# Optimization experiments

Measured on AMD Instinct MI355X. Metric: run time of the kernel, lower is better.

## Reference

```python
import jax, jax.numpy as jnp
import numpy as np

B, L, R = 4, 2048, 1024        # batch, seq_len, residual_dim
HID, EXP, K = 64, 2, 3          # hidden_dim, expansion_factor, conv_kernel_size
D = HID * EXP                   # ssm_input_dim = 128
N = HID                         # SSM state size = 64


def setup_inputs() -> dict:
    key = jax.random.key(0)
    ks = jax.random.split(key, 16)
    g = lambda k, s: jax.random.normal(k, s, dtype=jnp.float32) * 0.02
    inp = {
        "up_x":   jax.random.normal(ks[0], (B, L, R), dtype=jnp.float32),
        "W_up":   g(ks[1], (R, 2 * D)),
        "b_up":   g(ks[2], (2 * D,)),
        "conv_w": g(ks[3], (D, K)),          # depthwise Conv1d weight [C,1,K] squeezed
        "conv_b": g(ks[4], (D,)),
        "W_delta": g(ks[5], (D, D)),
        "b_delta": g(ks[6], (D,)),
        "W_B":    g(ks[7], (D, N)),
        "b_B":    g(ks[8], (N,)),
        "W_C":    g(ks[9], (D, N)),
        "b_C":    g(ks[10], (N,)),
        "A_log":  jnp.log(jnp.broadcast_to(jnp.arange(1, N + 1, dtype=jnp.float32), (D, N))),
        "D_skip": jnp.ones((D,), dtype=jnp.float32),
        "W_down": g(ks[11], (D, R)),
        "b_down": g(ks[12], (R,)),
    }
    return inp


def reference(up_x, W_up, b_up, conv_w, conv_b, W_delta, b_delta,
              W_B, b_B, W_C, b_C, A_log, D_skip, W_down, b_down):
    Lq = up_x.shape[1]
    u = up_x @ W_up + b_up                               # [B,L,2D]
    left, right = jnp.split(u, 2, axis=-1)               # each [B,L,D]

    # causal depthwise conv (pad left K-1, truncate to L)
    xp = jnp.pad(left, ((0, 0), (K - 1, 0), (0, 0)))     # [B,L+K-1,D]
    conv = sum(conv_w[:, k] * xp[:, k:k + Lq, :] for k in range(K)) + conv_b
    x = jax.nn.silu(conv)                                # [B,L,D]

    # S6 selective scan
    delta = jax.nn.softplus(x @ W_delta + b_delta)       # [B,L,D]
    Bm = x @ W_B + b_B                                   # [B,L,N]
    Cm = x @ W_C + b_C                                   # [B,L,N]
    A = -jnp.exp(A_log)                                  # [D,N]
    dA = jnp.exp(delta[..., None] * A)                   # [B,L,D,N]
    dBx = delta[..., None] * Bm[:, :, None, :] * x[..., None]  # [B,L,D,N]

    def step(h, inputs):
        dA_t, dBx_t, C_t = inputs                        # [B,D,N],[B,D,N],[B,N]
        h = dA_t * h + dBx_t
        y_t = jnp.einsum('bdn,bn->bd', h, C_t)
        return h, y_t

    h0 = jnp.zeros((up_x.shape[0], D, N), dtype=x.dtype)
    _, ys = jax.lax.scan(step, h0, (jnp.swapaxes(dA, 0, 1),
                                    jnp.swapaxes(dBx, 0, 1),
                                    jnp.swapaxes(Cm, 0, 1)))
    y = jnp.swapaxes(ys, 0, 1) + D_skip * x              # [B,L,D]

    gated = y * jax.nn.silu(right)                       # SiLU gate
    return gated @ W_down + b_down                       # [B,L,R]
```

## Files before the change

### kernel.cpp

```cpp
#include <hip/hip_runtime.h>
#include <math.h>

#define B_ 4
#define L_ 2048
#define R_ 1024
#define D_ 128
#define N_ 64
#define TWO_D 256
#define M_ (B_*L_)

#define LNC 6
#define NC 64

#define LSTR 68
#define LSTRX 136

typedef __attribute__((ext_vector_type(8))) short bf16x8;
typedef __attribute__((ext_vector_type(4))) float f32x4;

__device__ __forceinline__ float silu_f(float z) {
    return z / (1.0f + __expf(-z));
}

__device__ __forceinline__ float softplus_f(float z) {
    return fmaxf(z, 0.0f) + log1pf(__expf(-fabsf(z)));
}

__device__ __forceinline__ short f2bf(float f) {
    union { float f; unsigned int u; } v; v.f = f;
    unsigned int r = v.u + 0x7FFF + ((v.u >> 16) & 1);
    return (short)(r >> 16);
}

__device__ __forceinline__ bf16x8 pack8(float4 a, float4 b) {
    bf16x8 r;
    r[0] = f2bf(a.x); r[1] = f2bf(a.y); r[2] = f2bf(a.z); r[3] = f2bf(a.w);
    r[4] = f2bf(b.x); r[5] = f2bf(b.y); r[6] = f2bf(b.z); r[7] = f2bf(b.w);
    return r;
}

__global__ __launch_bounds__(256) void gemm_up_splitk(
    const float* __restrict__ A,
    const float* __restrict__ W,
    float* __restrict__ P0,
    float* __restrict__ P1)
{
    __shared__ short Al[64 * LSTR];
    __shared__ short Bl[64 * LSTR];

    int lid = blockIdx.x;
    int xcd = lid & 7;
    int slot = lid >> 3;
    int bm = xcd * 16 + (slot >> 3);
    int r3 = slot & 7;
    int bn = r3 & 3;
    int split = r3 >> 2;
    float* P = split ? P1 : P0;
    int k0 = split * 512;

    int tid = threadIdx.x;
    int w = tid >> 6, l = tid & 63;
    int lm = l & 15, q = l >> 4;
    int wm = (w & 1) * 32, wn = (w >> 1) * 32;

    f32x4 acc00 = {0,0,0,0}, acc01 = {0,0,0,0}, acc10 = {0,0,0,0}, acc11 = {0,0,0,0};

    int ar = tid >> 2, ak = (tid & 3) * 8;
    int bcol = tid & 63, bk = (tid >> 6) * 8;

    const float* Ag = A + (size_t)(bm * 64 + ar) * 1024 + k0 + ak;
    const float* Wg = W + (size_t)k0 * TWO_D + (size_t)bn * 64 + bcol;

    for (int kt = 0; kt < 512; kt += 32) {
        float4 a0 = *(const float4*)(Ag + kt);
        float4 a1 = *(const float4*)(Ag + kt + 4);
        *(bf16x8*)&Al[ar * LSTR + ak] = pack8(a0, a1);

        float w0 = Wg[(size_t)(kt + bk + 0) * TWO_D];
        float w1 = Wg[(size_t)(kt + bk + 1) * TWO_D];
        float w2 = Wg[(size_t)(kt + bk + 2) * TWO_D];
        float w3 = Wg[(size_t)(kt + bk + 3) * TWO_D];
        float w4 = Wg[(size_t)(kt + bk + 4) * TWO_D];
        float w5 = Wg[(size_t)(kt + bk + 5) * TWO_D];
        float w6 = Wg[(size_t)(kt + bk + 6) * TWO_D];
        float w7 = Wg[(size_t)(kt + bk + 7) * TWO_D];
        *(bf16x8*)&Bl[bcol * LSTR + bk] =
            pack8(make_float4(w0, w1, w2, w3), make_float4(w4, w5, w6, w7));

        __syncthreads();

        bf16x8 af0 = *(bf16x8*)&Al[(wm + lm) * LSTR + q * 8];
        bf16x8 af1 = *(bf16x8*)&Al[(wm + 16 + lm) * LSTR + q * 8];
        bf16x8 bf0 = *(bf16x8*)&Bl[(wn + lm) * LSTR + q * 8];
        bf16x8 bf1 = *(bf16x8*)&Bl[(wn + 16 + lm) * LSTR + q * 8];

        acc00 = __builtin_amdgcn_mfma_f32_16x16x32_bf16(af0, bf0, acc00, 0, 0, 0);
        acc01 = __builtin_amdgcn_mfma_f32_16x16x32_bf16(af0, bf1, acc01, 0, 0, 0);
        acc10 = __builtin_amdgcn_mfma_f32_16x16x32_bf16(af1, bf0, acc10, 0, 0, 0);
        acc11 = __builtin_amdgcn_mfma_f32_16x16x32_bf16(af1, bf1, acc11, 0, 0, 0);

        __syncthreads();
    }

    #pragma unroll
    for (int i = 0; i < 4; i++) {
        int r0 = bm * 64 + wm + q * 4 + i;
        int r1 = r0 + 16;
        int c0 = bn * 64 + wn + lm;
        int c1 = c0 + 16;
        P[(size_t)r0 * TWO_D + c0] = acc00[i];
        P[(size_t)r0 * TWO_D + c1] = acc01[i];
        P[(size_t)r1 * TWO_D + c0] = acc10[i];
        P[(size_t)r1 * TWO_D + c1] = acc11[i];
    }
}

__global__ __launch_bounds__(256) void convproj_mfma(
    const float* __restrict__ P0,
    const float* __restrict__ P1,
    const float* __restrict__ b_up,
    const float* __restrict__ conv_w,
    const float* __restrict__ conv_b,
    const float* __restrict__ W_delta, const float* __restrict__ b_delta,
    const float* __restrict__ W_B,     const float* __restrict__ b_B,
    const float* __restrict__ W_C,     const float* __restrict__ b_C,
    float* __restrict__ x,
    float* __restrict__ u,
    float* __restrict__ delta,
    float* __restrict__ Bm,
    float* __restrict__ Cm)
{
    __shared__ float uu[66 * 128];
    __shared__ short Xl[64 * LSTRX];
    __shared__ short Bl[64 * LSTR];

    int lid = blockIdx.x;
    int xcd = lid & 7;
    int slot = lid >> 3;
    int bm = xcd * 16 + (slot >> 2);
    int bn = slot & 3;
    int tid = threadIdx.x;

    bool seq_start = (bm & 31) == 0;

    #pragma unroll
    for (int i = 0; i < 9; i++) {
        int fi = tid + i * 256;
        if (fi < 2112) {
            int row = fi >> 5;
            int c4 = (fi & 31) * 4;
            int gr = bm * 64 + row - 2;
            float4 v;
            if (seq_start && row < 2) {
                v = make_float4(0.f, 0.f, 0.f, 0.f);
            } else {
                size_t gi = (size_t)gr * TWO_D + c4;
                float4 p0 = *(const float4*)&P0[gi];
                float4 p1 = *(const float4*)&P1[gi];
                float4 bb = *(const float4*)&b_up[c4];
                v = make_float4(p0.x + p1.x + bb.x, p0.y + p1.y + bb.y,
                                p0.z + p1.z + bb.z, p0.w + p1.w + bb.w);
            }
            *(float4*)&uu[fi * 4] = v;
        }
    }

    if (bn == 1) {
        #pragma unroll
        for (int i = 0; i < 8; i++) {
            int fi = tid + i * 256;
            int row = fi >> 5;
            int c4 = (fi & 31) * 4 + 128;
            int gr = bm * 64 + row;
            size_t gi = (size_t)gr * TWO_D + c4;
            float4 p0 = *(const float4*)&P0[gi];
            float4 p1 = *(const float4*)&P1[gi];
            float4 bb = *(const float4*)&b_up[c4];
            *(float4*)&u[gi] = make_float4(p0.x + p1.x + bb.x, p0.y + p1.y + bb.y,
                                           p0.z + p1.z + bb.z, p0.w + p1.w + bb.w);
        }
    }
    __syncthreads();

    #pragma unroll
    for (int i = 0; i < 8; i++) {
        int fi = tid + i * 256;
        int row = fi >> 5;
        int c4 = (fi & 31) * 4;
        float4 v2 = *(const float4*)&uu[(row + 2) * 128 + c4];
        float4 v1 = *(const float4*)&uu[(row + 1) * 128 + c4];
        float4 v0 = *(const float4*)&uu[(row + 0) * 128 + c4];
        float4 z;
        {
            float w0 = conv_w[(c4 + 0) * 3 + 0], w1 = conv_w[(c4 + 0) * 3 + 1], w2 = conv_w[(c4 + 0) * 3 + 2];
            z.x = silu_f(fmaf(w0, v0.x, fmaf(w1, v1.x, fmaf(w2, v2.x, conv_b[c4 + 0]))));
        }
        {
            float w0 = conv_w[(c4 + 1) * 3 + 0], w1 = conv_w[(c4 + 1) * 3 + 1], w2 = conv_w[(c4 + 1) * 3 + 2];
            z.y = silu_f(fmaf(w0, v0.y, fmaf(w1, v1.y, fmaf(w2, v2.y, conv_b[c4 + 1]))));
        }
        {
            float w0 = conv_w[(c4 + 2) * 3 + 0], w1 = conv_w[(c4 + 2) * 3 + 1], w2 = conv_w[(c4 + 2) * 3 + 2];
            z.z = silu_f(fmaf(w0, v0.z, fmaf(w1, v1.z, fmaf(w2, v2.z, conv_b[c4 + 2]))));
        }
        {
            float w0 = conv_w[(c4 + 3) * 3 + 0], w1 = conv_w[(c4 + 3) * 3 + 1], w2 = conv_w[(c4 + 3) * 3 + 2];
            z.w = silu_f(fmaf(w0, v0.w, fmaf(w1, v1.w, fmaf(w2, v2.w, conv_b[c4 + 3]))));
        }
        short4 zb;
        zb.x = f2bf(z.x); zb.y = f2bf(z.y); zb.z = f2bf(z.z); zb.w = f2bf(z.w);
        *(short4*)&Xl[row * LSTRX + c4] = zb;
        if (bn == 0) {
            int gr = bm * 64 + row;
            *(float4*)&x[(size_t)gr * D_ + c4] = z;
        }
    }

    const float* Wsel; const float* bsel; int wstride;
    if (bn < 2)       { Wsel = W_delta + bn * 64; bsel = b_delta + bn * 64; wstride = 128; }
    else if (bn == 2) { Wsel = W_B;               bsel = b_B;               wstride = 64;  }
    else              { Wsel = W_C;               bsel = b_C;               wstride = 64;  }

    int w = tid >> 6, l = tid & 63;
    int lm = l & 15, q = l >> 4;
    int wm = (w & 1) * 32, wn = (w >> 1) * 32;

    f32x4 acc00 = {0,0,0,0}, acc01 = {0,0,0,0}, acc10 = {0,0,0,0}, acc11 = {0,0,0,0};

    int bcol = tid & 63, bk = (tid >> 6) * 8;
    const float* Wg = Wsel + bcol;

    __syncthreads();

    for (int kt = 0; kt < 128; kt += 32) {
        float w0 = Wg[(size_t)(kt + bk + 0) * wstride];
        float w1 = Wg[(size_t)(kt + bk + 1) * wstride];
        float w2 = Wg[(size_t)(kt + bk + 2) * wstride];
        float w3 = Wg[(size_t)(kt + bk + 3) * wstride];
        float w4 = Wg[(size_t)(kt + bk + 4) * wstride];
        float w5 = Wg[(size_t)(kt + bk + 5) * wstride];
        float w6 = Wg[(size_t)(kt + bk + 6) * wstride];
        float w7 = Wg[(size_t)(kt + bk + 7) * wstride];
        *(bf16x8*)&Bl[bcol * LSTR + bk] =
            pack8(make_float4(w0, w1, w2, w3), make_float4(w4, w5, w6, w7));

        __syncthreads();

        bf16x8 af0 = *(bf16x8*)&Xl[(wm + lm) * LSTRX + kt + q * 8];
        bf16x8 af1 = *(bf16x8*)&Xl[(wm + 16 + lm) * LSTRX + kt + q * 8];
        bf16x8 bf0 = *(bf16x8*)&Bl[(wn + lm) * LSTR + q * 8];
        bf16x8 bf1 = *(bf16x8*)&Bl[(wn + 16 + lm) * LSTR + q * 8];

        acc00 = __builtin_amdgcn_mfma_f32_16x16x32_bf16(af0, bf0, acc00, 0, 0, 0);
        acc01 = __builtin_amdgcn_mfma_f32_16x16x32_bf16(af0, bf1, acc01, 0, 0, 0);
        acc10 = __builtin_amdgcn_mfma_f32_16x16x32_bf16(af1, bf0, acc10, 0, 0, 0);
        acc11 = __builtin_amdgcn_mfma_f32_16x16x32_bf16(af1, bf1, acc11, 0, 0, 0);

        __syncthreads();
    }

    #pragma unroll
    for (int i = 0; i < 4; i++) {
        int r0 = bm * 64 + wm + q * 4 + i;
        int r1 = r0 + 16;
        int c0 = wn + lm;
        int c1 = c0 + 16;
        float v00 = acc00[i] + bsel[c0];
        float v01 = acc01[i] + bsel[c1];
        float v10 = acc10[i] + bsel[c0];
        float v11 = acc11[i] + bsel[c1];
        if (bn < 2) {
            int cc0 = bn * 64 + c0, cc1 = bn * 64 + c1;
            delta[(size_t)r0 * D_ + cc0] = softplus_f(v00);
            delta[(size_t)r0 * D_ + cc1] = softplus_f(v01);
            delta[(size_t)r1 * D_ + cc0] = softplus_f(v10);
            delta[(size_t)r1 * D_ + cc1] = softplus_f(v11);
        } else if (bn == 2) {
            Bm[(size_t)r0 * N_ + c0] = v00;
            Bm[(size_t)r0 * N_ + c1] = v01;
            Bm[(size_t)r1 * N_ + c0] = v10;
            Bm[(size_t)r1 * N_ + c1] = v11;
        } else {
            Cm[(size_t)r0 * N_ + c0] = v00;
            Cm[(size_t)r0 * N_ + c1] = v01;
            Cm[(size_t)r1 * N_ + c0] = v10;
            Cm[(size_t)r1 * N_ + c1] = v11;
        }
    }
}

__global__ __launch_bounds__(256) void scan_sumA(
    const float* __restrict__ delta,
    const float* __restrict__ x,
    const float* __restrict__ Bm,
    const float* __restrict__ A_log,
    float* __restrict__ ch_aprod,
    float* __restrict__ ch_h)
{
    constexpr int TCt = L_ >> LNC;

    int wid = blockIdx.x * 4 + (threadIdx.x >> 6);
    int l = threadIdx.x & 63;
    int g = l >> 4, j = l & 15;
    int c = wid & (NC - 1);
    int dq = (wid >> LNC) & 31;
    int b = wid >> (LNC + 5);
    int d = dq * 4 + g;

    const float LOG2E = 1.44269504089f;
    float4 Ar = *(const float4*)&A_log[d * N_ + j * 4];
    float Ai0 = -__expf(Ar.x) * LOG2E;
    float Ai1 = -__expf(Ar.y) * LOG2E;
    float Ai2 = -__expf(Ar.z) * LOG2E;
    float Ai3 = -__expf(Ar.w) * LOG2E;

    size_t row0 = (size_t)b * L_ + c * TCt;
    const float* dp = delta + row0 * D_ + d;
    const float* xp = x     + row0 * D_ + d;
    const float* bp = Bm    + row0 * N_ + j * 4;

    float h0 = 0, h1 = 0, h2 = 0, h3 = 0;
    float S = 0;

    #pragma unroll 8
    for (int t = 0; t < TCt; t++) {
        float dl = dp[t * D_];
        float xv = xp[t * D_];
        float4 bv = *(const float4*)&bp[t * N_];
        float e0 = exp2f(dl * Ai0);
        float e1 = exp2f(dl * Ai1);
        float e2 = exp2f(dl * Ai2);
        float e3 = exp2f(dl * Ai3);
        float dbx = dl * xv;
        h0 = fmaf(e0, h0, dbx * bv.x);
        h1 = fmaf(e1, h1, dbx * bv.y);
        h2 = fmaf(e2, h2, dbx * bv.z);
        h3 = fmaf(e3, h3, dbx * bv.w);
        S += dl;
    }

    size_t ci = (((size_t)b * D_ + d) * NC + c) * N_ + j * 4;
    *(float4*)&ch_aprod[ci] = make_float4(exp2f(Ai0 * S), exp2f(Ai1 * S),
                                          exp2f(Ai2 * S), exp2f(Ai3 * S));
    *(float4*)&ch_h[ci]     = make_float4(h0, h1, h2, h3);
}

__global__ __launch_bounds__(256) void scan_prefix(
    float* __restrict__ aprod_hin,
    const float* __restrict__ ch_h)
{
    int idx = blockIdx.x * 256 + threadIdx.x;
    int n = idx & 63;
    int rest = idx >> 6;
    size_t base = (size_t)rest * NC * N_ + n;
    float h = 0.0f;
    #pragma unroll 8
    for (int c = 0; c < NC; c++) {
        size_t o = base + (size_t)c * N_;
        float a  = aprod_hin[o];
        float hh = ch_h[o];
        aprod_hin[o] = h;
        h = fmaf(a, h, hh);
    }
}

__global__ __launch_bounds__(256) void scan_outB(
    const float* __restrict__ delta,
    const float* __restrict__ x,
    const float* __restrict__ Bm,
    const float* __restrict__ Cm,
    const float* __restrict__ A_log,
    const float* __restrict__ D_skip,
    const float* __restrict__ hin,
    float* __restrict__ y)
{
    constexpr int TCt = L_ >> LNC;

    int wid = blockIdx.x * 4 + (threadIdx.x >> 6);
    int l = threadIdx.x & 63;
    int g = l >> 4, j = l & 15;
    int c = wid & (NC - 1);
    int dq = (wid >> LNC) & 31;
    int b = wid >> (LNC + 5);
    int d = dq * 4 + g;

    const float LOG2E = 1.44269504089f;
    float4 Ar = *(const float4*)&A_log[d * N_ + j * 4];
    float Ai0 = -__expf(Ar.x) * LOG2E;
    float Ai1 = -__expf(Ar.y) * LOG2E;
    float Ai2 = -__expf(Ar.z) * LOG2E;
    float Ai3 = -__expf(Ar.w) * LOG2E;
    float dsk = D_skip[d];

    float4 hv = *(const float4*)&hin[(((size_t)b * D_ + d) * NC + c) * N_ + j * 4];
    float h0 = hv.x, h1 = hv.y, h2 = hv.z, h3 = hv.w;

    size_t row0 = (size_t)b * L_ + c * TCt;
    const float* dp = delta + row0 * D_ + d;
    const float* xp = x     + row0 * D_ + d;
    const float* bp = Bm    + row0 * N_ + j * 4;
    const float* cp = Cm    + row0 * N_ + j * 4;
    float*       yp = y     + row0 * D_ + d;

    #pragma unroll 8
    for (int t = 0; t < TCt; t++) {
        float dl = dp[t * D_];
        float xv = xp[t * D_];
        float4 bv = *(const float4*)&bp[t * N_];
        float4 cv = *(const float4*)&cp[t * N_];
        float e0 = exp2f(dl * Ai0);
        float e1 = exp2f(dl * Ai1);
        float e2 = exp2f(dl * Ai2);
        float e3 = exp2f(dl * Ai3);
        float dbx = dl * xv;
        h0 = fmaf(e0, h0, dbx * bv.x);
        h1 = fmaf(e1, h1, dbx * bv.y);
        h2 = fmaf(e2, h2, dbx * bv.z);
        h3 = fmaf(e3, h3, dbx * bv.w);
        float p = fmaf(h0, cv.x, fmaf(h1, cv.y, fmaf(h2, cv.z, h3 * cv.w)));
        p += __shfl_xor(p, 1, 64);
        p += __shfl_xor(p, 2, 64);
        p += __shfl_xor(p, 4, 64);
        p += __shfl_xor(p, 8, 64);
        if (j == 0) yp[t * D_] = fmaf(dsk, xv, p);
    }
}

__global__ __launch_bounds__(256) void gemm_down_mfma(
    const float* __restrict__ y,
    const float* __restrict__ u,
    const float* __restrict__ W,
    const float* __restrict__ bias,
    float* __restrict__ out)
{
    __shared__ short Al[64 * LSTR];
    __shared__ short Bl[64 * LSTR];

    int lid = blockIdx.x;
    int xcd = lid & 7;
    int slot = lid >> 3;
    int bm = xcd * 16 + (slot >> 4);
    int bn = slot & 15;

    int tid = threadIdx.x;
    int w = tid >> 6, l = tid & 63;
    int lm = l & 15, q = l >> 4;
    int wm = (w & 1) * 32, wn = (w >> 1) * 32;

    f32x4 acc00 = {0,0,0,0}, acc01 = {0,0,0,0}, acc10 = {0,0,0,0}, acc11 = {0,0,0,0};

    int ar = tid >> 2, ak = (tid & 3) * 8;
    int bcol = tid & 63, bk = (tid >> 6) * 8;

    const float* Yg = y + (size_t)(bm * 64 + ar) * D_ + ak;
    const float* Ug = u + (size_t)(bm * 64 + ar) * TWO_D + D_ + ak;
    const float* Wg = W + (size_t)bn * 64 + bcol;

    for (int kt = 0; kt < 128; kt += 32) {
        float4 y0 = *(const float4*)(Yg + kt);
        float4 y1 = *(const float4*)(Yg + kt + 4);
        float4 g0 = *(const float4*)(Ug + kt);
        float4 g1 = *(const float4*)(Ug + kt + 4);
        float4 a0 = make_float4(y0.x * silu_f(g0.x), y0.y * silu_f(g0.y),
                                y0.z * silu_f(g0.z), y0.w * silu_f(g0.w));
        float4 a1 = make_float4(y1.x * silu_f(g1.x), y1.y * silu_f(g1.y),
                                y1.z * silu_f(g1.z), y1.w * silu_f(g1.w));
        *(bf16x8*)&Al[ar * LSTR + ak] = pack8(a0, a1);

        float w0 = Wg[(size_t)(kt + bk + 0) * R_];
        float w1 = Wg[(size_t)(kt + bk + 1) * R_];
        float w2 = Wg[(size_t)(kt + bk + 2) * R_];
        float w3 = Wg[(size_t)(kt + bk + 3) * R_];
        float w4 = Wg[(size_t)(kt + bk + 4) * R_];
        float w5 = Wg[(size_t)(kt + bk + 5) * R_];
        float w6 = Wg[(size_t)(kt + bk + 6) * R_];
        float w7 = Wg[(size_t)(kt + bk + 7) * R_];
        *(bf16x8*)&Bl[bcol * LSTR + bk] =
            pack8(make_float4(w0, w1, w2, w3), make_float4(w4, w5, w6, w7));

        __syncthreads();

        bf16x8 af0 = *(bf16x8*)&Al[(wm + lm) * LSTR + q * 8];
        bf16x8 af1 = *(bf16x8*)&Al[(wm + 16 + lm) * LSTR + q * 8];
        bf16x8 bf0 = *(bf16x8*)&Bl[(wn + lm) * LSTR + q * 8];
        bf16x8 bf1 = *(bf16x8*)&Bl[(wn + 16 + lm) * LSTR + q * 8];

        acc00 = __builtin_amdgcn_mfma_f32_16x16x32_bf16(af0, bf0, acc00, 0, 0, 0);
        acc01 = __builtin_amdgcn_mfma_f32_16x16x32_bf16(af0, bf1, acc01, 0, 0, 0);
        acc10 = __builtin_amdgcn_mfma_f32_16x16x32_bf16(af1, bf0, acc10, 0, 0, 0);
        acc11 = __builtin_amdgcn_mfma_f32_16x16x32_bf16(af1, bf1, acc11, 0, 0, 0);

        __syncthreads();
    }

    #pragma unroll
    for (int i = 0; i < 4; i++) {
        int r0 = bm * 64 + wm + q * 4 + i;
        int r1 = r0 + 16;
        int c0 = bn * 64 + wn + lm;
        int c1 = c0 + 16;
        out[(size_t)r0 * R_ + c0] = acc00[i] + bias[c0];
        out[(size_t)r0 * R_ + c1] = acc01[i] + bias[c1];
        out[(size_t)r1 * R_ + c0] = acc10[i] + bias[c0];
        out[(size_t)r1 * R_ + c1] = acc11[i] + bias[c1];
    }
}

extern "C" void kernel_launch(void* const* d_in, const int* in_sizes, int n_in,
                              void* d_out, int out_size, void* d_ws, size_t ws_size,
                              hipStream_t stream)
{
    const float* up_x    = (const float*)d_in[0];
    const float* W_up    = (const float*)d_in[1];
    const float* b_up    = (const float*)d_in[2];
    const float* conv_w  = (const float*)d_in[3];
    const float* conv_b  = (const float*)d_in[4];
    const float* W_delta = (const float*)d_in[5];
    const float* b_delta = (const float*)d_in[6];
    const float* W_B     = (const float*)d_in[7];
    const float* b_B     = (const float*)d_in[8];
    const float* W_C     = (const float*)d_in[9];
    const float* b_C     = (const float*)d_in[10];
    const float* A_log   = (const float*)d_in[11];
    const float* D_skip  = (const float*)d_in[12];
    const float* W_down  = (const float*)d_in[13];
    const float* b_down  = (const float*)d_in[14];

    float* out = (float*)d_out;
    float* ws  = (float*)d_ws;

    float* u     = ws;
    float* x     = u + (size_t)M_ * TWO_D;
    float* delta = x + (size_t)M_ * D_;
    float* Bm    = delta + (size_t)M_ * D_;
    float* Cm    = Bm + (size_t)M_ * N_;
    float* y     = Cm + (size_t)M_ * N_;
    float* ch_aprod = y + (size_t)M_ * D_;
    float* ch_h  = ch_aprod + (size_t)B_ * D_ * NC * N_;
    float* P0    = ch_h + (size_t)B_ * D_ * NC * N_;
    float* P1    = P0 + (size_t)M_ * TWO_D;

    gemm_up_splitk<<<1024, 256, 0, stream>>>(up_x, W_up, P0, P1);

    convproj_mfma<<<512, 256, 0, stream>>>(
        P0, P1, b_up, conv_w, conv_b,
        W_delta, b_delta, W_B, b_B, W_C, b_C,
        x, u, delta, Bm, Cm);

    scan_sumA<<<(B_ * (D_ / 4) * NC) / 4, 256, 0, stream>>>(
        delta, x, Bm, A_log, ch_aprod, ch_h);
    scan_prefix<<<(B_ * D_ * N_) / 256, 256, 0, stream>>>(
        ch_aprod, ch_h);
    scan_outB<<<(B_ * (D_ / 4) * NC) / 4, 256, 0, stream>>>(
        delta, x, Bm, Cm, A_log, D_skip, ch_aprod, y);

    gemm_down_mfma<<<16 * (M_ / 64), 256, 0, stream>>>(
        y, u, W_down, b_down, out);
}
```

Baseline: 217.2 us.

## Fuse SiLU gating into scan output, enlarge up-GEMM tile, remap scan blocks

The SiLU gate and the bf16 conversion now run at the end of scan_outB. Each block stages its y values in shared memory, then writes a bf16 gated tensor, so gemm_down only loads packed bf16 and no longer reads y and u in fp32. gemm_up_splitk now uses 128-row tiles with each wave computing 32x64, which halves the grid and improves reuse of the W tile. The scan blocks are remapped so the four waves in a block share a chunk and a group of channels, and silu/softplus switch to fast rcp/log intrinsics at a small cost in accuracy.

```diff
diff --git a/kernel.cpp b/kernel.cpp
--- a/kernel.cpp
+++ b/kernel.cpp
@@ -19,11 +19,11 @@
 typedef __attribute__((ext_vector_type(4))) float f32x4;
 
 __device__ __forceinline__ float silu_f(float z) {
-    return z / (1.0f + __expf(-z));
+    return z * __builtin_amdgcn_rcpf(1.0f + __expf(-z));
 }
 
 __device__ __forceinline__ float softplus_f(float z) {
-    return fmaxf(z, 0.0f) + log1pf(__expf(-fabsf(z)));
+    return fmaxf(z, 0.0f) + __logf(1.0f + __expf(-fabsf(z)));
 }
 
 __device__ __forceinline__ short f2bf(float f) {
@@ -45,13 +45,13 @@
     float* __restrict__ P0,
     float* __restrict__ P1)
 {
-    __shared__ short Al[64 * LSTR];
+    __shared__ short Al[128 * LSTR];
     __shared__ short Bl[64 * LSTR];
 
     int lid = blockIdx.x;
     int xcd = lid & 7;
     int slot = lid >> 3;
-    int bm = xcd * 16 + (slot >> 3);
+    int bm = xcd * 8 + (slot >> 3);
     int r3 = slot & 7;
     int bn = r3 & 3;
     int split = r3 >> 2;
@@ -61,20 +61,28 @@
     int tid = threadIdx.x;
     int w = tid >> 6, l = tid & 63;
     int lm = l & 15, q = l >> 4;
-    int wm = (w & 1) * 32, wn = (w >> 1) * 32;
-
-    f32x4 acc00 = {0,0,0,0}, acc01 = {0,0,0,0}, acc10 = {0,0,0,0}, acc11 = {0,0,0,0};
-
-    int ar = tid >> 2, ak = (tid & 3) * 8;
+    int wm = w * 32;
+
+    f32x4 acc[2][4];
+    #pragma unroll
+    for (int i = 0; i < 2; i++)
+        #pragma unroll
+        for (int f = 0; f < 4; f++)
+            acc[i][f] = (f32x4){0.f, 0.f, 0.f, 0.f};
+
+    int ar = tid >> 1, ak = (tid & 1) * 16;
     int bcol = tid & 63, bk = (tid >> 6) * 8;
 
-    const float* Ag = A + (size_t)(bm * 64 + ar) * 1024 + k0 + ak;
+    const float* Ag = A + (size_t)(bm * 128 + ar) * 1024 + k0 + ak;
     const float* Wg = W + (size_t)k0 * TWO_D + (size_t)bn * 64 + bcol;
 
     for (int kt = 0; kt < 512; kt += 32) {
         float4 a0 = *(const float4*)(Ag + kt);
         float4 a1 = *(const float4*)(Ag + kt + 4);
-        *(bf16x8*)&Al[ar * LSTR + ak] = pack8(a0, a1);
+        float4 a2 = *(const float4*)(Ag + kt + 8);
+        float4 a3 = *(const float4*)(Ag + kt + 12);
+        *(bf16x8*)&Al[ar * LSTR + ak]     = pack8(a0, a1);
+        *(bf16x8*)&Al[ar * LSTR + ak + 8] = pack8(a2, a3);
 
         float w0 = Wg[(size_t)(kt + bk + 0) * TWO_D];
         float w1 = Wg[(size_t)(kt + bk + 1) * TWO_D];
@@ -91,28 +99,30 @@
 
         bf16x8 af0 = *(bf16x8*)&Al[(wm + lm) * LSTR + q * 8];
         bf16x8 af1 = *(bf16x8*)&Al[(wm + 16 + lm) * LSTR + q * 8];
-        bf16x8 bf0 = *(bf16x8*)&Bl[(wn + lm) * LSTR + q * 8];
-        bf16x8 bf1 = *(bf16x8*)&Bl[(wn + 16 + lm) * LSTR + q * 8];
-
-        acc00 = __builtin_amdgcn_mfma_f32_16x16x32_bf16(af0, bf0, acc00, 0, 0, 0);
-        acc01 = __builtin_amdgcn_mfma_f32_16x16x32_bf16(af0, bf1, acc01, 0, 0, 0);
-        acc10 = __builtin_amdgcn_mfma_f32_16x16x32_bf16(af1, bf0, acc10, 0, 0, 0);
-        acc11 = __builtin_amdgcn_mfma_f32_16x16x32_bf16(af1, bf1, acc11, 0, 0, 0);
+        bf16x8 bfr[4];
+        #pragma unroll
+        for (int f = 0; f < 4; f++)
+            bfr[f] = *(bf16x8*)&Bl[(f * 16 + lm) * LSTR + q * 8];
+
+        #pragma unroll
+        for (int f = 0; f < 4; f++) {
+            acc[0][f] = __builtin_amdgcn_mfma_f32_16x16x32_bf16(af0, bfr[f], acc[0][f], 0, 0, 0);
+            acc[1][f] = __builtin_amdgcn_mfma_f32_16x16x32_bf16(af1, bfr[f], acc[1][f], 0, 0, 0);
+        }
 
         __syncthreads();
     }
 
     #pragma unroll
-    for (int i = 0; i < 4; i++) {
-        int r0 = bm * 64 + wm + q * 4 + i;
-        int r1 = r0 + 16;
-        int c0 = bn * 64 + wn + lm;
-        int c1 = c0 + 16;
-        P[(size_t)r0 * TWO_D + c0] = acc00[i];
-        P[(size_t)r0 * TWO_D + c1] = acc01[i];
-        P[(size_t)r1 * TWO_D + c0] = acc10[i];
-        P[(size_t)r1 * TWO_D + c1] = acc11[i];
-    }
+    for (int i = 0; i < 2; i++)
+        #pragma unroll
+        for (int f = 0; f < 4; f++)
+            #pragma unroll
+            for (int e = 0; e < 4; e++) {
+                int row = bm * 128 + wm + i * 16 + q * 4 + e;
+                int col = bn * 64 + f * 16 + lm;
+                P[(size_t)row * TWO_D + col] = acc[i][f][e];
+            }
 }
 
 __global__ __launch_bounds__(256) void convproj_mfma(
@@ -299,12 +309,14 @@
 {
     constexpr int TCt = L_ >> LNC;
 
-    int wid = blockIdx.x * 4 + (threadIdx.x >> 6);
+    int blk = blockIdx.x;
+    int c = blk & (NC - 1);
+    int dqg = (blk >> LNC) & 7;
+    int b = blk >> (LNC + 3);
+    int wv = threadIdx.x >> 6;
     int l = threadIdx.x & 63;
     int g = l >> 4, j = l & 15;
-    int c = wid & (NC - 1);
-    int dq = (wid >> LNC) & 31;
-    int b = wid >> (LNC + 5);
+    int dq = dqg * 4 + wv;
     int d = dq * 4 + g;
 
     const float LOG2E = 1.44269504089f;
@@ -372,16 +384,20 @@
     const float* __restrict__ A_log,
     const float* __restrict__ D_skip,
     const float* __restrict__ hin,
-    float* __restrict__ y)
+    const float* __restrict__ u,
+    short* __restrict__ gated)
 {
     constexpr int TCt = L_ >> LNC;
-
-    int wid = blockIdx.x * 4 + (threadIdx.x >> 6);
+    __shared__ float yl[TCt * 16];
+
+    int blk = blockIdx.x;
+    int c = blk & (NC - 1);
+    int dqg = (blk >> LNC) & 7;
+    int b = blk >> (LNC + 3);
+    int wv = threadIdx.x >> 6;
     int l = threadIdx.x & 63;
     int g = l >> 4, j = l & 15;
-    int c = wid & (NC - 1);
-    int dq = (wid >> LNC) & 31;
-    int b = wid >> (LNC + 5);
+    int dq = dqg * 4 + wv;
     int d = dq * 4 + g;
 
     const float LOG2E = 1.44269504089f;
@@ -400,7 +416,6 @@
     const float* xp = x     + row0 * D_ + d;
     const float* bp = Bm    + row0 * N_ + j * 4;
     const float* cp = Cm    + row0 * N_ + j * 4;
-    float*       yp = y     + row0 * D_ + d;
 
     #pragma unroll 8
     for (int t = 0; t < TCt; t++) {
@@ -422,13 +437,29 @@
         p += __shfl_xor(p, 2, 64);
         p += __shfl_xor(p, 4, 64);
         p += __shfl_xor(p, 8, 64);
-        if (j == 0) yp[t * D_] = fmaf(dsk, xv, p);
+        if (j == 0) yl[t * 16 + wv * 4 + g] = fmaf(dsk, xv, p);
+    }
+
+    __syncthreads();
+
+    int tid = threadIdx.x;
+    if (tid < 128) {
+        int t = tid >> 2;
+        int c4 = (tid & 3) * 4;
+        size_t row = row0 + t;
+        float4 yv = *(float4*)&yl[t * 16 + c4];
+        float4 gv = *(const float4*)&u[row * TWO_D + 128 + dqg * 16 + c4];
+        short4 o;
+        o.x = f2bf(yv.x * silu_f(gv.x));
+        o.y = f2bf(yv.y * silu_f(gv.y));
+        o.z = f2bf(yv.z * silu_f(gv.z));
+        o.w = f2bf(yv.w * silu_f(gv.w));
+        *(short4*)&gated[row * D_ + dqg * 16 + c4] = o;
     }
 }
 
 __global__ __launch_bounds__(256) void gemm_down_mfma(
-    const float* __restrict__ y,
-    const float* __restrict__ u,
+    const short* __restrict__ gated,
     const float* __restrict__ W,
     const float* __restrict__ bias,
     float* __restrict__ out)
@@ -452,20 +483,12 @@
     int ar = tid >> 2, ak = (tid & 3) * 8;
     int bcol = tid & 63, bk = (tid >> 6) * 8;
 
-    const float* Yg = y + (size_t)(bm * 64 + ar) * D_ + ak;
-    const float* Ug = u + (size_t)(bm * 64 + ar) * TWO_D + D_ + ak;
+    const short* Gg = gated + (size_t)(bm * 64 + ar) * D_ + ak;
     const float* Wg = W + (size_t)bn * 64 + bcol;
 
     for (int kt = 0; kt < 128; kt += 32) {
-        float4 y0 = *(const float4*)(Yg + kt);
-        float4 y1 = *(const float4*)(Yg + kt + 4);
-        float4 g0 = *(const float4*)(Ug + kt);
-        float4 g1 = *(const float4*)(Ug + kt + 4);
-        float4 a0 = make_float4(y0.x * silu_f(g0.x), y0.y * silu_f(g0.y),
-                                y0.z * silu_f(g0.z), y0.w * silu_f(g0.w));
-        float4 a1 = make_float4(y1.x * silu_f(g1.x), y1.y * silu_f(g1.y),
-                                y1.z * silu_f(g1.z), y1.w * silu_f(g1.w));
-        *(bf16x8*)&Al[ar * LSTR + ak] = pack8(a0, a1);
+        bf16x8 av = *(const bf16x8*)(Gg + kt);
+        *(bf16x8*)&Al[ar * LSTR + ak] = av;
 
         float w0 = Wg[(size_t)(kt + bk + 0) * R_];
         float w1 = Wg[(size_t)(kt + bk + 1) * R_];
@@ -534,26 +557,27 @@
     float* delta = x + (size_t)M_ * D_;
     float* Bm    = delta + (size_t)M_ * D_;
     float* Cm    = Bm + (size_t)M_ * N_;
-    float* y     = Cm + (size_t)M_ * N_;
-    float* ch_aprod = y + (size_t)M_ * D_;
+    float* yslot = Cm + (size_t)M_ * N_;
+    float* ch_aprod = yslot + (size_t)M_ * D_;
     float* ch_h  = ch_aprod + (size_t)B_ * D_ * NC * N_;
     float* P0    = ch_h + (size_t)B_ * D_ * NC * N_;
     float* P1    = P0 + (size_t)M_ * TWO_D;
-
-    gemm_up_splitk<<<1024, 256, 0, stream>>>(up_x, W_up, P0, P1);
+    short* gated = (short*)yslot;
+
+    gemm_up_splitk<<<512, 256, 0, stream>>>(up_x, W_up, P0, P1);
 
     convproj_mfma<<<512, 256, 0, stream>>>(
         P0, P1, b_up, conv_w, conv_b,
         W_delta, b_delta, W_B, b_B, W_C, b_C,
         x, u, delta, Bm, Cm);
 
-    scan_sumA<<<(B_ * (D_ / 4) * NC) / 4, 256, 0, stream>>>(
+    scan_sumA<<<2048, 256, 0, stream>>>(
         delta, x, Bm, A_log, ch_aprod, ch_h);
     scan_prefix<<<(B_ * D_ * N_) / 256, 256, 0, stream>>>(
         ch_aprod, ch_h);
-    scan_outB<<<(B_ * (D_ / 4) * NC) / 4, 256, 0, stream>>>(
-        delta, x, Bm, Cm, A_log, D_skip, ch_aprod, y);
-
-    gemm_down_mfma<<<16 * (M_ / 64), 256, 0, stream>>>(
-        y, u, W_down, b_down, out);
-}
+    scan_outB<<<2048, 256, 0, stream>>>(
+        delta, x, Bm, Cm, A_log, D_skip, ch_aprod, u, gated);
+
+    gemm_down_mfma<<<2048, 256, 0, stream>>>(
+        gated, W_down, b_down, out);
+}
```

After: 210.4 us. 1.03x faster.
